# Optimization experiments

Measured on AMD Instinct MI355X. Metric: run time of the kernel, lower is better.

## Reference

```python
import jax, jax.numpy as jnp
import numpy as np

DROPOUT_P = 0.2


def setup_inputs() -> dict:
    key = jax.random.key(0)
    kq, kk, kv = jax.random.split(key, 3)
    B, Sq, Sk, D, Dv = 4, 4096, 4096, 64, 64
    return {
        "query": jax.random.normal(kq, (B, Sq, D), dtype=jnp.float32),
        "key": jax.random.normal(kk, (B, Sk, D), dtype=jnp.float32),
        "value": jax.random.normal(kv, (B, Sk, Dv), dtype=jnp.float32),
        "inv_scale_factor": 8,
    }


def reference(query, key, value, inv_scale_factor):
    # qk = Q K^T / inv_scale_factor  -> [B, Sq, Sk]
    scaled_qk = jnp.einsum("bqd,bkd->bqk", query, key) / inv_scale_factor
    probs = jax.nn.softmax(scaled_qk, axis=-1)
    # dropout (train mode, p=0.2) with a fixed key for determinism
    keep = jax.random.bernoulli(jax.random.key(42), 1.0 - DROPOUT_P, probs.shape)
    probs = jnp.where(keep, probs / (1.0 - DROPOUT_P), 0.0)
    # [B, Sq, Sk] @ [B, Sk, Dv] -> [B, Sq, Dv]
    return jnp.einsum("bqk,bkv->bqv", probs, value)
```

## Files before the change

### kernel.cpp

```cpp
#include <hip/hip_runtime.h>
#include <stdint.h>

#define S_LEN 4096
#define D_DIM 64
#define KBLK  64
#define QBLK  64
#define NBATCH 4
#define ROWSTRIDE 66

typedef __attribute__((ext_vector_type(8))) short bf16x8;
typedef __attribute__((ext_vector_type(4))) float f32x4;

__device__ __forceinline__ uint32_t f2bf(float f) {
    uint32_t u = __float_as_uint(f);
    return (u + 0x7FFFu + ((u >> 16) & 1u)) >> 16;
}
__device__ __forceinline__ uint32_t pack2bf(float lo, float hi) {
    return f2bf(lo) | (f2bf(hi) << 16);
}
__device__ __forceinline__ uint32_t rotl32(uint32_t x, int n) {
    return (x << n) | (x >> (32 - n));
}

__device__ __forceinline__ uint32_t threefry_xor(uint32_t idx) {
    const uint32_t k0 = 0u, k1 = 42u;
    const uint32_t k2 = 0x1BD11BDAu ^ k0 ^ k1;
    uint32_t x0 = k0;
    uint32_t x1 = idx + k1;
#define TFR(r) { x0 += x1; x1 = rotl32(x1, (r)); x1 ^= x0; }
    TFR(13) TFR(15) TFR(26) TFR(6)
    x0 += k1; x1 += k2 + 1u;
    TFR(17) TFR(29) TFR(16) TFR(24)
    x0 += k2; x1 += k0 + 2u;
    TFR(13) TFR(15) TFR(26) TFR(6)
    x0 += k0; x1 += k1 + 3u;
    TFR(17) TFR(29) TFR(16) TFR(24)
    x0 += k1; x1 += k2 + 4u;
    TFR(13) TFR(15) TFR(26) TFR(6)
    x0 += k2; x1 += k0 + 5u;
#undef TFR
    return x0 ^ x1;
}

#define KEEP_THRESH 0xCCCCCE00u

template <bool DIRECT>
__global__ void attn_fwd_kernel(const float* __restrict__ Qp,
                                const float* __restrict__ Kp,
                                const float* __restrict__ Vp,
                                const int* __restrict__ isf,
                                float* __restrict__ outp,
                                int seg_tiles) {
    const int tid  = threadIdx.x;
    const int w    = tid >> 6;
    const int lane = tid & 63;
    const int g    = lane >> 4;
    const int lq   = lane & 15;
    const int b    = blockIdx.y;
    const int qwave = blockIdx.x * QBLK + w * 16;

    __shared__ __align__(16) unsigned char smem[24576];
    unsigned char* Kl = smem;
    unsigned char* Vt = smem + 8192;
    unsigned char* Pl = smem + 16384 + w * 2048;

    float fv;
    {
        int iv = isf[0];
        if (iv >= 1 && iv <= (1 << 20)) fv = (float)iv;
        else {
            float f = __int_as_float(iv);
            fv = (f > 1.0e-3f && f < 1.0e6f) ? f : 8.0f;
        }
    }
    const float sc = 1.0f / fv;

    bf16x8 qf[2];
    {
        const float* qp = Qp + (size_t)(b * S_LEN + qwave + lq) * D_DIM + 8 * g;
        #pragma unroll
        for (int h = 0; h < 2; ++h) {
            float4 a = *(const float4*)(qp + 32 * h);
            float4 c = *(const float4*)(qp + 32 * h + 4);
            bf16x8 f;
            f[0] = (short)f2bf(a.x * sc); f[1] = (short)f2bf(a.y * sc);
            f[2] = (short)f2bf(a.z * sc); f[3] = (short)f2bf(a.w * sc);
            f[4] = (short)f2bf(c.x * sc); f[5] = (short)f2bf(c.y * sc);
            f[6] = (short)f2bf(c.z * sc); f[7] = (short)f2bf(c.w * sc);
            qf[h] = f;
        }
    }

    f32x4 acc[4];
    #pragma unroll
    for (int nt = 0; nt < 4; ++nt) { acc[nt][0]=0.f; acc[nt][1]=0.f; acc[nt][2]=0.f; acc[nt][3]=0.f; }
    float mrun = -3.0e38f, lrun = 0.0f;

    const float* Kb = Kp + (size_t)b * S_LEN * D_DIM;
    const float* Vb = Vp + (size_t)b * S_LEN * D_DIM;

    const int kt0 = blockIdx.z * seg_tiles;
    for (int kt = kt0; kt < kt0 + seg_tiles; ++kt) {
        const int kbase = kt * KBLK;
        __syncthreads();

        #pragma unroll
        for (int i = 0; i < 4; ++i) {
            int p4 = i * 256 + tid;
            int r  = p4 >> 4, c4 = p4 & 15;
            float4 v = *(const float4*)(Kb + (size_t)(kbase + r) * D_DIM + c4 * 4);
            uint2 wv; wv.x = pack2bf(v.x, v.y); wv.y = pack2bf(v.z, v.w);
            *(uint2*)(Kl + ((r * 128 + c4 * 8) ^ ((r & 7) << 4))) = wv;
        }
        #pragma unroll
        for (int i = 0; i < 2; ++i) {
            int pp = i * 256 + tid;
            int kp = pp >> 4, d4 = (pp & 15) * 4;
            const float* vp = Vb + (size_t)(kbase + 2 * kp) * D_DIM + d4;
            float4 a = *(const float4*)vp;
            float4 c = *(const float4*)(vp + D_DIM);
            *(uint32_t*)(Vt + (((d4 + 0) * 128 + kp * 4) ^ (((d4 + 0) & 7) << 4))) = pack2bf(a.x, c.x);
            *(uint32_t*)(Vt + (((d4 + 1) * 128 + kp * 4) ^ (((d4 + 1) & 7) << 4))) = pack2bf(a.y, c.y);
            *(uint32_t*)(Vt + (((d4 + 2) * 128 + kp * 4) ^ (((d4 + 2) & 7) << 4))) = pack2bf(a.z, c.z);
            *(uint32_t*)(Vt + (((d4 + 3) * 128 + kp * 4) ^ (((d4 + 3) & 7) << 4))) = pack2bf(a.w, c.w);
        }
        __syncthreads();

        f32x4 s[4];
        #pragma unroll
        for (int mt = 0; mt < 4; ++mt) { s[mt][0]=0.f; s[mt][1]=0.f; s[mt][2]=0.f; s[mt][3]=0.f; }
        #pragma unroll
        for (int h = 0; h < 2; ++h) {
            #pragma unroll
            for (int mt = 0; mt < 4; ++mt) {
                int r = 16 * mt + lq;
                bf16x8 kf = *(const bf16x8*)(Kl + ((r * 128 + (4 * h + g) * 16) ^ ((r & 7) << 4)));
                s[mt] = __builtin_amdgcn_mfma_f32_16x16x32_bf16(kf, qf[h], s[mt], 0, 0, 0);
            }
        }

        float tmax = s[0][0];
        #pragma unroll
        for (int mt = 0; mt < 4; ++mt)
            #pragma unroll
            for (int r = 0; r < 4; ++r) tmax = fmaxf(tmax, s[mt][r]);
        tmax = fmaxf(tmax, __shfl_xor(tmax, 16));
        tmax = fmaxf(tmax, __shfl_xor(tmax, 32));
        float mnew = fmaxf(mrun, tmax);
        float pvv[4][4];
        float tsum = 0.f;
        #pragma unroll
        for (int mt = 0; mt < 4; ++mt)
            #pragma unroll
            for (int r = 0; r < 4; ++r) {
                float e = __expf(s[mt][r] - mnew);
                pvv[mt][r] = e; tsum += e;
            }
        tsum += __shfl_xor(tsum, 16);
        tsum += __shfl_xor(tsum, 32);
        float corr = __expf(mrun - mnew);
        lrun = lrun * corr + tsum;
        mrun = mnew;

        const uint32_t cbase = ((uint32_t)b << 24) + ((uint32_t)(qwave + lq) << 12) + (uint32_t)kbase;
        #pragma unroll
        for (int mt = 0; mt < 4; ++mt) {
            float pd[4];
            #pragma unroll
            for (int r = 0; r < 4; ++r) {
                uint32_t bits = threefry_xor(cbase + (uint32_t)(16 * mt + 4 * g + r));
                pd[r] = (bits < KEEP_THRESH) ? pvv[mt][r] : 0.0f;
            }
            uint2 pw; pw.x = pack2bf(pd[0], pd[1]); pw.y = pack2bf(pd[2], pd[3]);
            *(uint2*)(Pl + ((lq * 128 + (16 * mt + 4 * g) * 2) ^ ((lq & 7) << 4))) = pw;
        }

        asm volatile("" ::: "memory");

        float cr0 = __shfl(corr, 4 * g + 0);
        float cr1 = __shfl(corr, 4 * g + 1);
        float cr2 = __shfl(corr, 4 * g + 2);
        float cr3 = __shfl(corr, 4 * g + 3);
        #pragma unroll
        for (int nt = 0; nt < 4; ++nt) {
            acc[nt][0] *= cr0; acc[nt][1] *= cr1; acc[nt][2] *= cr2; acc[nt][3] *= cr3;
        }

        #pragma unroll
        for (int kk = 0; kk < 2; ++kk) {
            bf16x8 pf = *(const bf16x8*)(Pl + ((lq * 128 + kk * 64 + g * 16) ^ ((lq & 7) << 4)));
            #pragma unroll
            for (int nt = 0; nt < 4; ++nt) {
                int d = lq + 16 * nt;
                bf16x8 vf = *(const bf16x8*)(Vt + ((d * 128 + kk * 64 + g * 16) ^ ((d & 7) << 4)));
                acc[nt] = __builtin_amdgcn_mfma_f32_16x16x32_bf16(pf, vf, acc[nt], 0, 0, 0);
            }
        }
    }

    if (DIRECT) {
        float l0 = __shfl(lrun, 4 * g + 0);
        float l1 = __shfl(lrun, 4 * g + 1);
        float l2 = __shfl(lrun, 4 * g + 2);
        float l3 = __shfl(lrun, 4 * g + 3);
        float inv0 = 1.0f / (l0 * 0.8f);
        float inv1 = 1.0f / (l1 * 0.8f);
        float inv2 = 1.0f / (l2 * 0.8f);
        float inv3 = 1.0f / (l3 * 0.8f);
        float* Ob = outp + (size_t)b * S_LEN * D_DIM;
        #pragma unroll
        for (int nt = 0; nt < 4; ++nt) {
            int d = lq + 16 * nt;
            Ob[(size_t)(qwave + 4 * g + 0) * D_DIM + d] = acc[nt][0] * inv0;
            Ob[(size_t)(qwave + 4 * g + 1) * D_DIM + d] = acc[nt][1] * inv1;
            Ob[(size_t)(qwave + 4 * g + 2) * D_DIM + d] = acc[nt][2] * inv2;
            Ob[(size_t)(qwave + 4 * g + 3) * D_DIM + d] = acc[nt][3] * inv3;
        }
    } else {
        float* seg = outp + (size_t)blockIdx.z * NBATCH * S_LEN * ROWSTRIDE;
        size_t row0 = (size_t)b * S_LEN + qwave;
        if (g == 0) {
            float* p = seg + (row0 + lq) * ROWSTRIDE;
            p[0] = mrun; p[1] = lrun;
        }
        #pragma unroll
        for (int nt = 0; nt < 4; ++nt) {
            int d = lq + 16 * nt;
            seg[(row0 + 4 * g + 0) * ROWSTRIDE + 2 + d] = acc[nt][0];
            seg[(row0 + 4 * g + 1) * ROWSTRIDE + 2 + d] = acc[nt][1];
            seg[(row0 + 4 * g + 2) * ROWSTRIDE + 2 + d] = acc[nt][2];
            seg[(row0 + 4 * g + 3) * ROWSTRIDE + 2 + d] = acc[nt][3];
        }
    }
}

__global__ void combine_kernel(const float* __restrict__ ws, float* __restrict__ Op, int NS) {
    const int tid = threadIdx.x;
    const size_t row = (size_t)blockIdx.x * 4 + (tid >> 6);
    const int d = tid & 63;
    const size_t SEGF = (size_t)NBATCH * S_LEN * ROWSTRIDE;
    const size_t roff = row * ROWSTRIDE;

    float m = -3.0e38f;
    for (int s = 0; s < NS; ++s) m = fmaxf(m, ws[s * SEGF + roff]);
    float l = 0.f, o = 0.f;
    for (int s = 0; s < NS; ++s) {
        const float* p = ws + s * SEGF + roff;
        float scl = __expf(p[0] - m);
        l += scl * p[1];
        o += scl * p[2 + d];
    }
    Op[row * D_DIM + d] = o / (l * 0.8f);
}

extern "C" void kernel_launch(void* const* d_in, const int* in_sizes, int n_in,
                              void* d_out, int out_size, void* d_ws, size_t ws_size,
                              hipStream_t stream) {
    const float* Q = (const float*)d_in[0];
    const float* K = (const float*)d_in[1];
    const float* V = (const float*)d_in[2];
    const int* isf = (const int*)d_in[3];
    float* O = (float*)d_out;

    const size_t SEGB = (size_t)NBATCH * S_LEN * ROWSTRIDE * sizeof(float);
    int NS = 4;
    while (NS > 1 && ws_size < (size_t)NS * SEGB) NS >>= 1;

    if (NS >= 2) {
        dim3 grid1(S_LEN / QBLK, NBATCH, NS);
        attn_fwd_kernel<false><<<grid1, dim3(256), 0, stream>>>(
            Q, K, V, isf, (float*)d_ws, (S_LEN / KBLK) / NS);
        dim3 grid2((NBATCH * S_LEN) / 4);
        combine_kernel<<<grid2, dim3(256), 0, stream>>>((const float*)d_ws, O, NS);
    } else {
        dim3 grid(S_LEN / QBLK, NBATCH, 1);
        attn_fwd_kernel<true><<<grid, dim3(256), 0, stream>>>(
            Q, K, V, isf, O, S_LEN / KBLK);
    }
}
```

Measured before the change: 172.2 us.

## Use hardware bf16 pack, exp2 with folded log2e, alignbit rotates, more K splits

Replaces the software round-to-nearest bf16 conversion with the v_cvt_pk_bf16_f32 instruction and implements rotates with alignbit, which shortens the threefry dropout hash. The log2(e) factor is folded into the Q scaling so softmax can call the raw exp2 builtin directly. The split-K segment count rises from 4 to 8 when the workspace allows, adding parallelism in exchange for more combine traffic. Folding the scale before bf16 rounding slightly changes numerics.

```diff
diff --git a/kernel.cpp b/kernel.cpp
--- a/kernel.cpp
+++ b/kernel.cpp
@@ -11,15 +11,15 @@
 typedef __attribute__((ext_vector_type(8))) short bf16x8;
 typedef __attribute__((ext_vector_type(4))) float f32x4;
 
-__device__ __forceinline__ uint32_t f2bf(float f) {
-    uint32_t u = __float_as_uint(f);
-    return (u + 0x7FFFu + ((u >> 16) & 1u)) >> 16;
-}
-__device__ __forceinline__ uint32_t pack2bf(float lo, float hi) {
-    return f2bf(lo) | (f2bf(hi) << 16);
+#define LOG2E 1.4426950408889634f
+
+__device__ __forceinline__ uint32_t pk_bf16(float lo, float hi) {
+    uint32_t r;
+    asm("v_cvt_pk_bf16_f32 %0, %1, %2" : "=v"(r) : "v"(lo), "v"(hi));
+    return r;
 }
 __device__ __forceinline__ uint32_t rotl32(uint32_t x, int n) {
-    return (x << n) | (x >> (32 - n));
+    return __builtin_amdgcn_alignbit(x, x, 32 - n);
 }
 
 __device__ __forceinline__ uint32_t threefry_xor(uint32_t idx) {
@@ -73,7 +73,7 @@
             fv = (f > 1.0e-3f && f < 1.0e6f) ? f : 8.0f;
         }
     }
-    const float sc = 1.0f / fv;
+    const float sc = LOG2E / fv;
 
     bf16x8 qf[2];
     {
@@ -82,11 +82,15 @@
         for (int h = 0; h < 2; ++h) {
             float4 a = *(const float4*)(qp + 32 * h);
             float4 c = *(const float4*)(qp + 32 * h + 4);
+            uint32_t w0 = pk_bf16(a.x * sc, a.y * sc);
+            uint32_t w1 = pk_bf16(a.z * sc, a.w * sc);
+            uint32_t w2 = pk_bf16(c.x * sc, c.y * sc);
+            uint32_t w3 = pk_bf16(c.z * sc, c.w * sc);
             bf16x8 f;
-            f[0] = (short)f2bf(a.x * sc); f[1] = (short)f2bf(a.y * sc);
-            f[2] = (short)f2bf(a.z * sc); f[3] = (short)f2bf(a.w * sc);
-            f[4] = (short)f2bf(c.x * sc); f[5] = (short)f2bf(c.y * sc);
-            f[6] = (short)f2bf(c.z * sc); f[7] = (short)f2bf(c.w * sc);
+            f[0] = (short)(w0 & 0xFFFF); f[1] = (short)(w0 >> 16);
+            f[2] = (short)(w1 & 0xFFFF); f[3] = (short)(w1 >> 16);
+            f[4] = (short)(w2 & 0xFFFF); f[5] = (short)(w2 >> 16);
+            f[6] = (short)(w3 & 0xFFFF); f[7] = (short)(w3 >> 16);
             qf[h] = f;
         }
     }
@@ -109,7 +113,7 @@
             int p4 = i * 256 + tid;
             int r  = p4 >> 4, c4 = p4 & 15;
             float4 v = *(const float4*)(Kb + (size_t)(kbase + r) * D_DIM + c4 * 4);
-            uint2 wv; wv.x = pack2bf(v.x, v.y); wv.y = pack2bf(v.z, v.w);
+            uint2 wv; wv.x = pk_bf16(v.x, v.y); wv.y = pk_bf16(v.z, v.w);
             *(uint2*)(Kl + ((r * 128 + c4 * 8) ^ ((r & 7) << 4))) = wv;
         }
         #pragma unroll
@@ -119,10 +123,10 @@
             const float* vp = Vb + (size_t)(kbase + 2 * kp) * D_DIM + d4;
             float4 a = *(const float4*)vp;
             float4 c = *(const float4*)(vp + D_DIM);
-            *(uint32_t*)(Vt + (((d4 + 0) * 128 + kp * 4) ^ (((d4 + 0) & 7) << 4))) = pack2bf(a.x, c.x);
-            *(uint32_t*)(Vt + (((d4 + 1) * 128 + kp * 4) ^ (((d4 + 1) & 7) << 4))) = pack2bf(a.y, c.y);
-            *(uint32_t*)(Vt + (((d4 + 2) * 128 + kp * 4) ^ (((d4 + 2) & 7) << 4))) = pack2bf(a.z, c.z);
-            *(uint32_t*)(Vt + (((d4 + 3) * 128 + kp * 4) ^ (((d4 + 3) & 7) << 4))) = pack2bf(a.w, c.w);
+            *(uint32_t*)(Vt + (((d4 + 0) * 128 + kp * 4) ^ (((d4 + 0) & 7) << 4))) = pk_bf16(a.x, c.x);
+            *(uint32_t*)(Vt + (((d4 + 1) * 128 + kp * 4) ^ (((d4 + 1) & 7) << 4))) = pk_bf16(a.y, c.y);
+            *(uint32_t*)(Vt + (((d4 + 2) * 128 + kp * 4) ^ (((d4 + 2) & 7) << 4))) = pk_bf16(a.z, c.z);
+            *(uint32_t*)(Vt + (((d4 + 3) * 128 + kp * 4) ^ (((d4 + 3) & 7) << 4))) = pk_bf16(a.w, c.w);
         }
         __syncthreads();
 
@@ -153,12 +157,12 @@
         for (int mt = 0; mt < 4; ++mt)
             #pragma unroll
             for (int r = 0; r < 4; ++r) {
-                float e = __expf(s[mt][r] - mnew);
+                float e = __builtin_amdgcn_exp2f(s[mt][r] - mnew);
                 pvv[mt][r] = e; tsum += e;
             }
         tsum += __shfl_xor(tsum, 16);
         tsum += __shfl_xor(tsum, 32);
-        float corr = __expf(mrun - mnew);
+        float corr = __builtin_amdgcn_exp2f(mrun - mnew);
         lrun = lrun * corr + tsum;
         mrun = mnew;
 
@@ -171,7 +175,7 @@
                 uint32_t bits = threefry_xor(cbase + (uint32_t)(16 * mt + 4 * g + r));
                 pd[r] = (bits < KEEP_THRESH) ? pvv[mt][r] : 0.0f;
             }
-            uint2 pw; pw.x = pack2bf(pd[0], pd[1]); pw.y = pack2bf(pd[2], pd[3]);
+            uint2 pw; pw.x = pk_bf16(pd[0], pd[1]); pw.y = pk_bf16(pd[2], pd[3]);
             *(uint2*)(Pl + ((lq * 128 + (16 * mt + 4 * g) * 2) ^ ((lq & 7) << 4))) = pw;
         }
 
@@ -246,7 +250,7 @@
     float l = 0.f, o = 0.f;
     for (int s = 0; s < NS; ++s) {
         const float* p = ws + s * SEGF + roff;
-        float scl = __expf(p[0] - m);
+        float scl = __builtin_amdgcn_exp2f(p[0] - m);
         l += scl * p[1];
         o += scl * p[2 + d];
     }
@@ -263,7 +267,7 @@
     float* O = (float*)d_out;
 
     const size_t SEGB = (size_t)NBATCH * S_LEN * ROWSTRIDE * sizeof(float);
-    int NS = 4;
+    int NS = 8;
     while (NS > 1 && ws_size < (size_t)NS * SEGB) NS >>= 1;
 
     if (NS >= 2) {
```

Measured after the change: 162.2 us. -5.8%, faster.
